# Kernel optimization log

Hardware: AMD Instinct MI355X
Metric: run time of the kernel (lower is better)

## Reference

```python
import jax, jax.numpy as jnp
import numpy as np

N_NODES = 100000
N_EDGES = 1600000
D_FEAT = 64


def setup_inputs() -> dict:
    key = jax.random.key(0)
    k1, k2, k3 = jax.random.split(key, 3)
    features = jax.random.normal(k1, (N_NODES, D_FEAT), dtype=jnp.float32)
    row = jax.random.randint(k2, (N_EDGES,), 0, N_NODES, dtype=jnp.int64 if jax.config.jax_enable_x64 else jnp.int32)
    col = jax.random.randint(k3, (N_EDGES,), 0, N_NODES, dtype=jnp.int64 if jax.config.jax_enable_x64 else jnp.int32)
    return {"features": features, "row": row, "col": col}


def reference(features, row, col):
    # adj @ H  ==  segment-sum of H[col] grouped by row (COO SpMM)
    n = features.shape[0]
    gathered = features[col]                                  # [E, d] irregular gather
    summed = jax.ops.segment_sum(gathered, row, num_segments=n)  # [N, d]
    # deg = clip(adj.sum(1), 1, None) -> per-row nonzero count
    ones = jnp.ones((row.shape[0],), dtype=features.dtype)
    deg = jax.ops.segment_sum(ones, row, num_segments=n)
    deg = jnp.clip(deg, 1.0, None)
    agg = summed / deg[:, None]
    # combine: residual add
    return features + agg
```

## Files before the change

### kernel.cpp

```cpp
#include <hip/hip_runtime.h>

#define D_FEAT 64
#define RB 64
#define RBITS 6
#define CELLCAP 16
#define E_BLK 8192
#define TMAX 256
#define NBMAX2 1600
#define SCAP 2048
#define OVCAP 65536

__device__ inline unsigned short f2bf(float f) {
    unsigned u = __float_as_uint(f);
    u += 0x7FFFu + ((u >> 16) & 1u);
    return (unsigned short)(u >> 16);
}
__device__ inline float bf_lo(unsigned u) { return __uint_as_float(u << 16); }
__device__ inline float bf_hi(unsigned u) { return __uint_as_float(u & 0xFFFF0000u); }

__global__ __launch_bounds__(64)
void zero_kernel(int* __restrict__ p, int n) {
    int i = blockIdx.x * 64 + threadIdx.x;
    if (i < n) p[i] = 0;
}

__global__ __launch_bounds__(256)
void bin2_conv_kernel(const int* __restrict__ row, const int* __restrict__ col,
                      int* __restrict__ cnts,
                      int* __restrict__ slab,
                      int* __restrict__ ovfcnt,
                      int2* __restrict__ ovf,
                      int n_edges, int ebt, int nb,
                      const float* __restrict__ feat, unsigned short* __restrict__ feat_bf,
                      int n4) {
    int gb = blockIdx.x;
    int t = threadIdx.x;
    if (gb < ebt) {
        __shared__ int hist[NBMAX2];
        __shared__ int cur[NBMAX2];
        for (int i = t; i < nb; i += 256) { hist[i] = 0; cur[i] = 0; }
        __syncthreads();
        int e0 = gb * E_BLK, e1 = min(e0 + E_BLK, n_edges);
        for (int e = e0 + t; e < e1; e += 256)
            atomicAdd(&hist[row[e] >> RBITS], 1);
        __syncthreads();
        for (int i = t; i < nb; i += 256)
            cnts[(size_t)gb * nb + i] = hist[i];
        for (int e = e0 + t; e < e1; e += 256) {
            int r = row[e], c = col[e];
            int b = r >> RBITS;
            int pos = atomicAdd(&cur[b], 1);
            if (pos < CELLCAP) {
                slab[((size_t)b * ebt + gb) * CELLCAP + pos] = ((r & (RB - 1)) << 17) | c;
            } else {
                int op = atomicAdd(ovfcnt, 1);
                if (op < OVCAP) ovf[op] = make_int2(r, c);
            }
        }
    } else {
        int i = (gb - ebt) * 256 + t;
        if (i < n4) {
            float4 f = reinterpret_cast<const float4*>(feat)[i];
            ushort4 u;
            u.x = f2bf(f.x); u.y = f2bf(f.y); u.z = f2bf(f.z); u.w = f2bf(f.w);
            reinterpret_cast<ushort4*>(feat_bf)[i] = u;
        }
    }
}

template<int BF>
__global__ __launch_bounds__(256, 6)
void aggregate5_kernel(const float* __restrict__ feat,
                       const unsigned short* __restrict__ feat_bf,
                       const int* __restrict__ slab,
                       const int* __restrict__ cnts,
                       const int* __restrict__ ovfcnt,
                       const int2* __restrict__ ovf,
                       const int* __restrict__ row, const int* __restrict__ col,
                       float* __restrict__ out, int n_nodes, int n_edges,
                       int nb, int ebt) {
    __shared__ int cellc[TMAX];
    __shared__ int scol[SCAP];
    __shared__ int cnt[RB], csum[RB], cur[RB], ddeg[RB];
    __shared__ int sred[256];

    int b = blockIdx.x;
    int t = threadIdx.x;
    int w = t >> 6, lane = t & 63;
    int q = lane >> 3, sub = lane & 7;
    int rA = w * 16 + q;
    int rB = rA + 8;

    for (int i = t; i < ebt; i += 256) cellc[i] = cnts[(size_t)i * nb + b];
    if (t < RB) { cnt[t] = 0; ddeg[t] = 0; }
    __syncthreads();

    int pt = 0;
    for (int i = t; i < ebt; i += 256) pt += cellc[i];
    sred[t] = pt;
    __syncthreads();
    for (int o = 128; o > 0; o >>= 1) {
        if (t < o) sred[t] += sred[t + o];
        __syncthreads();
    }
    int btotal = sred[0];
    int rawoc = *ovfcnt;
    int oc = min(rawoc, OVCAP);
    bool fb = (btotal > SCAP) || (rawoc > OVCAP);

    float acc[16];
    #pragma unroll
    for (int k = 0; k < 16; ++k) acc[k] = 0.f;

#define GATHER(cv, o0)                                                         \
    do {                                                                       \
        if (BF) {                                                              \
            uint4 d = *reinterpret_cast<const uint4*>(                         \
                feat_bf + (size_t)(cv)*D_FEAT + sub * 8);                      \
            acc[o0+0] += bf_lo(d.x); acc[o0+1] += bf_hi(d.x);                  \
            acc[o0+2] += bf_lo(d.y); acc[o0+3] += bf_hi(d.y);                  \
            acc[o0+4] += bf_lo(d.z); acc[o0+5] += bf_hi(d.z);                  \
            acc[o0+6] += bf_lo(d.w); acc[o0+7] += bf_hi(d.w);                  \
        } else {                                                               \
            float4 x0 = *reinterpret_cast<const float4*>(                      \
                feat + (size_t)(cv)*D_FEAT + sub * 8);                         \
            float4 x1 = *reinterpret_cast<const float4*>(                      \
                feat + (size_t)(cv)*D_FEAT + sub * 8 + 4);                     \
            acc[o0+0] += x0.x; acc[o0+1] += x0.y;                              \
            acc[o0+2] += x0.z; acc[o0+3] += x0.w;                              \
            acc[o0+4] += x1.x; acc[o0+5] += x1.y;                              \
            acc[o0+6] += x1.z; acc[o0+7] += x1.w;                              \
        }                                                                      \
    } while (0)

    if (!fb) {
        int nslots = ebt * CELLCAP;
        const int* sp = slab + (size_t)b * nslots;
        for (int i = t; i < nslots; i += 256) {
            int cell = i >> 4, pos = i & 15;
            if (pos < min(cellc[cell], CELLCAP)) {
                int pk = sp[i];
                atomicAdd(&cnt[((unsigned)pk) >> 17], 1);
            }
        }
        for (int i = t; i < oc; i += 256) {
            int2 rc = ovf[i];
            if ((rc.x >> RBITS) == b) atomicAdd(&cnt[rc.x & (RB - 1)], 1);
        }
        __syncthreads();
        if (t < RB) csum[t] = cnt[t];
        __syncthreads();
        for (int o = 1; o < RB; o <<= 1) {
            int v = (t < RB && t >= o) ? csum[t - o] : 0;
            __syncthreads();
            if (t < RB) csum[t] += v;
            __syncthreads();
        }
        if (t < RB) { cur[t] = csum[t] - cnt[t]; ddeg[t] = cnt[t]; }
        __syncthreads();
        for (int i = t; i < nslots; i += 256) {
            int cell = i >> 4, pos = i & 15;
            if (pos < min(cellc[cell], CELLCAP)) {
                int pk = sp[i];
                int lr = ((unsigned)pk) >> 17;
                scol[atomicAdd(&cur[lr], 1)] = pk & 0x1FFFF;
            }
        }
        for (int i = t; i < oc; i += 256) {
            int2 rc = ovf[i];
            if ((rc.x >> RBITS) == b)
                scol[atomicAdd(&cur[rc.x & (RB - 1)], 1)] = rc.y;
        }
        __syncthreads();
        int cA = cnt[rA], sA = csum[rA] - cA;
        int cB = cnt[rB], sB = csum[rB] - cB;
        int m = max(cA, cB);
        for (int j = 0; j < m; ++j) {
            if (j < cA) { int c = scol[sA + j]; GATHER(c, 0); }
            if (j < cB) { int c = scol[sB + j]; GATHER(c, 8); }
        }
    } else {
        for (int base = 0; base < n_edges; base += SCAP) {
            int ce = min(SCAP, n_edges - base);
            if (t < RB) cnt[t] = 0;
            __syncthreads();
            for (int i = t; i < ce; i += 256) {
                int r = row[base + i];
                if ((r >> RBITS) == b) atomicAdd(&cnt[r & (RB - 1)], 1);
            }
            __syncthreads();
            if (t < RB) csum[t] = cnt[t];
            __syncthreads();
            for (int o = 1; o < RB; o <<= 1) {
                int v = (t < RB && t >= o) ? csum[t - o] : 0;
                __syncthreads();
                if (t < RB) csum[t] += v;
                __syncthreads();
            }
            if (t < RB) { cur[t] = csum[t] - cnt[t]; ddeg[t] += cnt[t]; }
            __syncthreads();
            for (int i = t; i < ce; i += 256) {
                int r = row[base + i];
                if ((r >> RBITS) == b)
                    scol[atomicAdd(&cur[r & (RB - 1)], 1)] = col[base + i];
            }
            __syncthreads();
            int cA = cnt[rA], sA = csum[rA] - cA;
            int cB = cnt[rB], sB = csum[rB] - cB;
            int m = max(cA, cB);
            for (int j = 0; j < m; ++j) {
                if (j < cA) { int c = scol[sA + j]; GATHER(c, 0); }
                if (j < cB) { int c = scol[sB + j]; GATHER(c, 8); }
            }
            __syncthreads();
        }
    }
    __syncthreads();

    {
        int r = b * RB + rA;
        if (r < n_nodes) {
            float inv = 1.0f / fmaxf((float)ddeg[rA], 1.0f);
            size_t off = (size_t)r * D_FEAT + sub * 8;
            float4 f0 = *reinterpret_cast<const float4*>(feat + off);
            float4 f1 = *reinterpret_cast<const float4*>(feat + off + 4);
            float4 o0, o1;
            o0.x = f0.x + acc[0] * inv; o0.y = f0.y + acc[1] * inv;
            o0.z = f0.z + acc[2] * inv; o0.w = f0.w + acc[3] * inv;
            o1.x = f1.x + acc[4] * inv; o1.y = f1.y + acc[5] * inv;
            o1.z = f1.z + acc[6] * inv; o1.w = f1.w + acc[7] * inv;
            *reinterpret_cast<float4*>(out + off) = o0;
            *reinterpret_cast<float4*>(out + off + 4) = o1;
        }
        r = b * RB + rB;
        if (r < n_nodes) {
            float inv = 1.0f / fmaxf((float)ddeg[rB], 1.0f);
            size_t off = (size_t)r * D_FEAT + sub * 8;
            float4 f0 = *reinterpret_cast<const float4*>(feat + off);
            float4 f1 = *reinterpret_cast<const float4*>(feat + off + 4);
            float4 o0, o1;
            o0.x = f0.x + acc[8]  * inv; o0.y = f0.y + acc[9]  * inv;
            o0.z = f0.z + acc[10] * inv; o0.w = f0.w + acc[11] * inv;
            o1.x = f1.x + acc[12] * inv; o1.y = f1.y + acc[13] * inv;
            o1.z = f1.z + acc[14] * inv; o1.w = f1.w + acc[15] * inv;
            *reinterpret_cast<float4*>(out + off) = o0;
            *reinterpret_cast<float4*>(out + off + 4) = o1;
        }
    }
#undef GATHER
}

extern "C" void kernel_launch(void* const* d_in, const int* in_sizes, int n_in,
                              void* d_out, int out_size, void* d_ws, size_t ws_size,
                              hipStream_t stream) {
    const float* feat = (const float*)d_in[0];
    const int* row = (const int*)d_in[1];
    const int* col = (const int*)d_in[2];
    float* out = (float*)d_out;

    const int n_nodes = in_sizes[0] / D_FEAT;
    const int n_edges = in_sizes[1];
    const int nb = (n_nodes + RB - 1) / RB;
    const int ebt = (n_edges + E_BLK - 1) / E_BLK;
    const int n4 = n_nodes * D_FEAT / 4;

    size_t slab_bytes = (size_t)nb * ebt * CELLCAP * 4;
    size_t cnts_bytes = (size_t)ebt * nb * 4;
    size_t ovf_bytes  = (size_t)OVCAP * 8;
    size_t bf_bytes   = (size_t)n_nodes * D_FEAT * 2;

    size_t lean_need = slab_bytes + cnts_bytes + ovf_bytes + 512;
    size_t fat_need  = lean_need + ((bf_bytes + 63) & ~(size_t)63);
    bool fat = (ws_size >= fat_need);

    char* ws = (char*)d_ws;
    size_t p = 0;
    int* slab = (int*)(ws + p); p += slab_bytes;
    int* cnts = (int*)(ws + p); p += cnts_bytes;
    int2* ovf = (int2*)(ws + p); p += ovf_bytes;
    int* ovfcnt = (int*)(ws + p); p += 64;
    p = (p + 63) & ~(size_t)63;
    unsigned short* feat_bf = nullptr;
    if (fat) { feat_bf = (unsigned short*)(ws + p); }

    zero_kernel<<<1, 64, 0, stream>>>(ovfcnt, 1);

    {
        int conv_blocks = fat ? (n4 + 255) / 256 : 0;
        bin2_conv_kernel<<<ebt + conv_blocks, 256, 0, stream>>>(
            row, col, cnts, slab, ovfcnt, ovf, n_edges, ebt, nb,
            feat, feat_bf, fat ? n4 : 0);
    }
    if (fat) {
        aggregate5_kernel<1><<<nb, 256, 0, stream>>>(
            feat, feat_bf, slab, cnts, ovfcnt, ovf, row, col,
            out, n_nodes, n_edges, nb, ebt);
    } else {
        aggregate5_kernel<0><<<nb, 256, 0, stream>>>(
            feat, nullptr, slab, cnts, ovfcnt, ovf, row, col,
            out, n_nodes, n_edges, nb, ebt);
    }
}
```

Measured before the change: 151.8 us.

## Drop binning histogram pass and balance row gathers across edges with shuffle reduction

The binning kernel now runs 1024 threads per block and uses its final per-bin cursor values as the cell counts, which removes the separate histogram pass over row indices. The aggregate kernel moves to 512 threads. Each wave now processes one row at a time, with 8 lane groups splitting that row's edges and combining partial sums through cross-lane shuffles. The previous scheme gave each thread group fixed rows and iterated to the larger row degree. The new mapping targets load imbalance between rows and lets each row issue more gathers in parallel, at the cost of shuffle reductions and a larger block. The fallback path now accumulates in the output buffer across chunks.

```diff
diff --git a/kernel.cpp b/kernel.cpp
--- a/kernel.cpp
+++ b/kernel.cpp
@@ -24,8 +24,8 @@
     if (i < n) p[i] = 0;
 }
 
-__global__ __launch_bounds__(256)
-void bin2_conv_kernel(const int* __restrict__ row, const int* __restrict__ col,
+__global__ __launch_bounds__(1024)
+void bin3_conv_kernel(const int* __restrict__ row, const int* __restrict__ col,
                       int* __restrict__ cnts,
                       int* __restrict__ slab,
                       int* __restrict__ ovfcnt,
@@ -36,17 +36,11 @@
     int gb = blockIdx.x;
     int t = threadIdx.x;
     if (gb < ebt) {
-        __shared__ int hist[NBMAX2];
         __shared__ int cur[NBMAX2];
-        for (int i = t; i < nb; i += 256) { hist[i] = 0; cur[i] = 0; }
+        for (int i = t; i < nb; i += 1024) cur[i] = 0;
         __syncthreads();
         int e0 = gb * E_BLK, e1 = min(e0 + E_BLK, n_edges);
-        for (int e = e0 + t; e < e1; e += 256)
-            atomicAdd(&hist[row[e] >> RBITS], 1);
-        __syncthreads();
-        for (int i = t; i < nb; i += 256)
-            cnts[(size_t)gb * nb + i] = hist[i];
-        for (int e = e0 + t; e < e1; e += 256) {
+        for (int e = e0 + t; e < e1; e += 1024) {
             int r = row[e], c = col[e];
             int b = r >> RBITS;
             int pos = atomicAdd(&cur[b], 1);
@@ -57,8 +51,11 @@
                 if (op < OVCAP) ovf[op] = make_int2(r, c);
             }
         }
+        __syncthreads();
+        for (int i = t; i < nb; i += 1024)
+            cnts[(size_t)gb * nb + i] = cur[i];
     } else {
-        int i = (gb - ebt) * 256 + t;
+        int i = (gb - ebt) * 1024 + t;
         if (i < n4) {
             float4 f = reinterpret_cast<const float4*>(feat)[i];
             ushort4 u;
@@ -69,8 +66,8 @@
 }
 
 template<int BF>
-__global__ __launch_bounds__(256, 6)
-void aggregate5_kernel(const float* __restrict__ feat,
+__global__ __launch_bounds__(512, 4)
+void aggregate6_kernel(const float* __restrict__ feat,
                        const unsigned short* __restrict__ feat_bf,
                        const int* __restrict__ slab,
                        const int* __restrict__ cnts,
@@ -82,24 +79,22 @@
     __shared__ int cellc[TMAX];
     __shared__ int scol[SCAP];
     __shared__ int cnt[RB], csum[RB], cur[RB], ddeg[RB];
-    __shared__ int sred[256];
+    __shared__ int sred[512];
 
     int b = blockIdx.x;
     int t = threadIdx.x;
     int w = t >> 6, lane = t & 63;
     int q = lane >> 3, sub = lane & 7;
-    int rA = w * 16 + q;
-    int rB = rA + 8;
-
-    for (int i = t; i < ebt; i += 256) cellc[i] = cnts[(size_t)i * nb + b];
+
+    for (int i = t; i < ebt; i += 512) cellc[i] = cnts[(size_t)i * nb + b];
     if (t < RB) { cnt[t] = 0; ddeg[t] = 0; }
     __syncthreads();
 
     int pt = 0;
-    for (int i = t; i < ebt; i += 256) pt += cellc[i];
+    for (int i = t; i < ebt; i += 512) pt += cellc[i];
     sred[t] = pt;
     __syncthreads();
-    for (int o = 128; o > 0; o >>= 1) {
+    for (int o = 256; o > 0; o >>= 1) {
         if (t < o) sred[t] += sred[t + o];
         __syncthreads();
     }
@@ -108,84 +103,115 @@
     int oc = min(rawoc, OVCAP);
     bool fb = (btotal > SCAP) || (rawoc > OVCAP);
 
-    float acc[16];
-    #pragma unroll
-    for (int k = 0; k < 16; ++k) acc[k] = 0.f;
-
-#define GATHER(cv, o0)                                                         \
+#define GATHER(cv, A)                                                          \
     do {                                                                       \
         if (BF) {                                                              \
             uint4 d = *reinterpret_cast<const uint4*>(                         \
                 feat_bf + (size_t)(cv)*D_FEAT + sub * 8);                      \
-            acc[o0+0] += bf_lo(d.x); acc[o0+1] += bf_hi(d.x);                  \
-            acc[o0+2] += bf_lo(d.y); acc[o0+3] += bf_hi(d.y);                  \
-            acc[o0+4] += bf_lo(d.z); acc[o0+5] += bf_hi(d.z);                  \
-            acc[o0+6] += bf_lo(d.w); acc[o0+7] += bf_hi(d.w);                  \
+            A[0] += bf_lo(d.x); A[1] += bf_hi(d.x);                            \
+            A[2] += bf_lo(d.y); A[3] += bf_hi(d.y);                            \
+            A[4] += bf_lo(d.z); A[5] += bf_hi(d.z);                            \
+            A[6] += bf_lo(d.w); A[7] += bf_hi(d.w);                            \
         } else {                                                               \
             float4 x0 = *reinterpret_cast<const float4*>(                      \
                 feat + (size_t)(cv)*D_FEAT + sub * 8);                         \
             float4 x1 = *reinterpret_cast<const float4*>(                      \
                 feat + (size_t)(cv)*D_FEAT + sub * 8 + 4);                     \
-            acc[o0+0] += x0.x; acc[o0+1] += x0.y;                              \
-            acc[o0+2] += x0.z; acc[o0+3] += x0.w;                              \
-            acc[o0+4] += x1.x; acc[o0+5] += x1.y;                              \
-            acc[o0+6] += x1.z; acc[o0+7] += x1.w;                              \
+            A[0] += x0.x; A[1] += x0.y; A[2] += x0.z; A[3] += x0.w;            \
+            A[4] += x1.x; A[5] += x1.y; A[6] += x1.z; A[7] += x1.w;            \
         }                                                                      \
     } while (0)
 
     if (!fb) {
         int nslots = ebt * CELLCAP;
         const int* sp = slab + (size_t)b * nslots;
-        for (int i = t; i < nslots; i += 256) {
+        for (int i = t; i < nslots; i += 512) {
+            int cell = i >> 4, pos = i & 15;
+            if (pos < min(cellc[cell], CELLCAP))
+                atomicAdd(&cnt[((unsigned)sp[i]) >> 17], 1);
+        }
+        for (int i = t; i < oc; i += 512) {
+            int2 rc = ovf[i];
+            if ((rc.x >> RBITS) == b) atomicAdd(&cnt[rc.x & (RB - 1)], 1);
+        }
+        __syncthreads();
+        if (t < RB) csum[t] = cnt[t];
+        __syncthreads();
+        for (int o = 1; o < RB; o <<= 1) {
+            int v = (t < RB && t >= o) ? csum[t - o] : 0;
+            __syncthreads();
+            if (t < RB) csum[t] += v;
+            __syncthreads();
+        }
+        if (t < RB) cur[t] = csum[t] - cnt[t];
+        __syncthreads();
+        for (int i = t; i < nslots; i += 512) {
             int cell = i >> 4, pos = i & 15;
             if (pos < min(cellc[cell], CELLCAP)) {
                 int pk = sp[i];
-                atomicAdd(&cnt[((unsigned)pk) >> 17], 1);
-            }
-        }
-        for (int i = t; i < oc; i += 256) {
-            int2 rc = ovf[i];
-            if ((rc.x >> RBITS) == b) atomicAdd(&cnt[rc.x & (RB - 1)], 1);
-        }
-        __syncthreads();
-        if (t < RB) csum[t] = cnt[t];
-        __syncthreads();
-        for (int o = 1; o < RB; o <<= 1) {
-            int v = (t < RB && t >= o) ? csum[t - o] : 0;
-            __syncthreads();
-            if (t < RB) csum[t] += v;
-            __syncthreads();
-        }
-        if (t < RB) { cur[t] = csum[t] - cnt[t]; ddeg[t] = cnt[t]; }
-        __syncthreads();
-        for (int i = t; i < nslots; i += 256) {
-            int cell = i >> 4, pos = i & 15;
-            if (pos < min(cellc[cell], CELLCAP)) {
-                int pk = sp[i];
-                int lr = ((unsigned)pk) >> 17;
-                scol[atomicAdd(&cur[lr], 1)] = pk & 0x1FFFF;
-            }
-        }
-        for (int i = t; i < oc; i += 256) {
+                scol[atomicAdd(&cur[((unsigned)pk) >> 17], 1)] = pk & 0x1FFFF;
+            }
+        }
+        for (int i = t; i < oc; i += 512) {
             int2 rc = ovf[i];
             if ((rc.x >> RBITS) == b)
                 scol[atomicAdd(&cur[rc.x & (RB - 1)], 1)] = rc.y;
         }
         __syncthreads();
-        int cA = cnt[rA], sA = csum[rA] - cA;
-        int cB = cnt[rB], sB = csum[rB] - cB;
-        int m = max(cA, cB);
-        for (int j = 0; j < m; ++j) {
-            if (j < cA) { int c = scol[sA + j]; GATHER(c, 0); }
-            if (j < cB) { int c = scol[sB + j]; GATHER(c, 8); }
+        #pragma unroll 2
+        for (int rr = 0; rr < 8; ++rr) {
+            int lr = w + rr * 8;
+            int r = b * RB + lr;
+            if (r >= n_nodes) continue;
+            int deg = cnt[lr];
+            int s0 = csum[lr] - deg;
+            float a0[8], a1[8];
+            #pragma unroll
+            for (int k = 0; k < 8; ++k) { a0[k] = 0.f; a1[k] = 0.f; }
+            for (int base = 0; base < deg; base += 16) {
+                int j0 = base + q, j1 = base + 8 + q;
+                int c0 = (j0 < deg) ? scol[s0 + j0] : -1;
+                int c1 = (j1 < deg) ? scol[s0 + j1] : -1;
+                if (c0 >= 0) GATHER(c0, a0);
+                if (c1 >= 0) GATHER(c1, a1);
+            }
+            #pragma unroll
+            for (int k = 0; k < 8; ++k) a0[k] += a1[k];
+            #pragma unroll
+            for (int k = 0; k < 8; ++k) {
+                a0[k] += __shfl_xor(a0[k], 8, 64);
+                a0[k] += __shfl_xor(a0[k], 16, 64);
+                a0[k] += __shfl_xor(a0[k], 32, 64);
+            }
+            if (q == 0) {
+                float inv = 1.0f / fmaxf((float)deg, 1.0f);
+                size_t off = (size_t)r * D_FEAT + sub * 8;
+                float4 f0 = *reinterpret_cast<const float4*>(feat + off);
+                float4 f1 = *reinterpret_cast<const float4*>(feat + off + 4);
+                float4 o0, o1;
+                o0.x = f0.x + a0[0] * inv; o0.y = f0.y + a0[1] * inv;
+                o0.z = f0.z + a0[2] * inv; o0.w = f0.w + a0[3] * inv;
+                o1.x = f1.x + a0[4] * inv; o1.y = f1.y + a0[5] * inv;
+                o1.z = f1.z + a0[6] * inv; o1.w = f1.w + a0[7] * inv;
+                *reinterpret_cast<float4*>(out + off) = o0;
+                *reinterpret_cast<float4*>(out + off + 4) = o1;
+            }
         }
     } else {
-        for (int base = 0; base < n_edges; base += SCAP) {
-            int ce = min(SCAP, n_edges - base);
+        for (int j = t; j < RB * 16; j += 512) {
+            int lr = j >> 4, r = b * RB + lr;
+            if (r < n_nodes) {
+                float4 z = make_float4(0.f, 0.f, 0.f, 0.f);
+                *reinterpret_cast<float4*>(out + (size_t)r * D_FEAT + (j & 15) * 4) = z;
+            }
+        }
+        __syncthreads();
+        for (int base0 = 0; base0 < n_edges; base0 += SCAP) {
+            int ce = min(SCAP, n_edges - base0);
             if (t < RB) cnt[t] = 0;
             __syncthreads();
-            for (int i = t; i < ce; i += 256) {
-                int r = row[base + i];
+            for (int i = t; i < ce; i += 512) {
+                int r = row[base0 + i];
                 if ((r >> RBITS) == b) atomicAdd(&cnt[r & (RB - 1)], 1);
             }
             __syncthreads();
@@ -199,52 +225,61 @@
             }
             if (t < RB) { cur[t] = csum[t] - cnt[t]; ddeg[t] += cnt[t]; }
             __syncthreads();
-            for (int i = t; i < ce; i += 256) {
-                int r = row[base + i];
+            for (int i = t; i < ce; i += 512) {
+                int r = row[base0 + i];
                 if ((r >> RBITS) == b)
-                    scol[atomicAdd(&cur[r & (RB - 1)], 1)] = col[base + i];
-            }
-            __syncthreads();
-            int cA = cnt[rA], sA = csum[rA] - cA;
-            int cB = cnt[rB], sB = csum[rB] - cB;
-            int m = max(cA, cB);
-            for (int j = 0; j < m; ++j) {
-                if (j < cA) { int c = scol[sA + j]; GATHER(c, 0); }
-                if (j < cB) { int c = scol[sB + j]; GATHER(c, 8); }
-            }
-            __syncthreads();
-        }
-    }
-    __syncthreads();
-
-    {
-        int r = b * RB + rA;
-        if (r < n_nodes) {
-            float inv = 1.0f / fmaxf((float)ddeg[rA], 1.0f);
-            size_t off = (size_t)r * D_FEAT + sub * 8;
-            float4 f0 = *reinterpret_cast<const float4*>(feat + off);
-            float4 f1 = *reinterpret_cast<const float4*>(feat + off + 4);
-            float4 o0, o1;
-            o0.x = f0.x + acc[0] * inv; o0.y = f0.y + acc[1] * inv;
-            o0.z = f0.z + acc[2] * inv; o0.w = f0.w + acc[3] * inv;
-            o1.x = f1.x + acc[4] * inv; o1.y = f1.y + acc[5] * inv;
-            o1.z = f1.z + acc[6] * inv; o1.w = f1.w + acc[7] * inv;
-            *reinterpret_cast<float4*>(out + off) = o0;
-            *reinterpret_cast<float4*>(out + off + 4) = o1;
-        }
-        r = b * RB + rB;
-        if (r < n_nodes) {
-            float inv = 1.0f / fmaxf((float)ddeg[rB], 1.0f);
-            size_t off = (size_t)r * D_FEAT + sub * 8;
-            float4 f0 = *reinterpret_cast<const float4*>(feat + off);
-            float4 f1 = *reinterpret_cast<const float4*>(feat + off + 4);
-            float4 o0, o1;
-            o0.x = f0.x + acc[8]  * inv; o0.y = f0.y + acc[9]  * inv;
-            o0.z = f0.z + acc[10] * inv; o0.w = f0.w + acc[11] * inv;
-            o1.x = f1.x + acc[12] * inv; o1.y = f1.y + acc[13] * inv;
-            o1.z = f1.z + acc[14] * inv; o1.w = f1.w + acc[15] * inv;
-            *reinterpret_cast<float4*>(out + off) = o0;
-            *reinterpret_cast<float4*>(out + off + 4) = o1;
+                    scol[atomicAdd(&cur[r & (RB - 1)], 1)] = col[base0 + i];
+            }
+            __syncthreads();
+            for (int rr = 0; rr < 8; ++rr) {
+                int lr = w + rr * 8;
+                int r = b * RB + lr;
+                if (r >= n_nodes) continue;
+                int deg = cnt[lr];
+                int s0 = csum[lr] - deg;
+                float a0[8], a1[8];
+                #pragma unroll
+                for (int k = 0; k < 8; ++k) { a0[k] = 0.f; a1[k] = 0.f; }
+                for (int base = 0; base < deg; base += 16) {
+                    int j0 = base + q, j1 = base + 8 + q;
+                    int c0 = (j0 < deg) ? scol[s0 + j0] : -1;
+                    int c1 = (j1 < deg) ? scol[s0 + j1] : -1;
+                    if (c0 >= 0) GATHER(c0, a0);
+                    if (c1 >= 0) GATHER(c1, a1);
+                }
+                #pragma unroll
+                for (int k = 0; k < 8; ++k) a0[k] += a1[k];
+                #pragma unroll
+                for (int k = 0; k < 8; ++k) {
+                    a0[k] += __shfl_xor(a0[k], 8, 64);
+                    a0[k] += __shfl_xor(a0[k], 16, 64);
+                    a0[k] += __shfl_xor(a0[k], 32, 64);
+                }
+                if (q == 0) {
+                    size_t off = (size_t)r * D_FEAT + sub * 8;
+                    float4 s0v = *reinterpret_cast<const float4*>(out + off);
+                    float4 s1v = *reinterpret_cast<const float4*>(out + off + 4);
+                    s0v.x += a0[0]; s0v.y += a0[1]; s0v.z += a0[2]; s0v.w += a0[3];
+                    s1v.x += a0[4]; s1v.y += a0[5]; s1v.z += a0[6]; s1v.w += a0[7];
+                    *reinterpret_cast<float4*>(out + off) = s0v;
+                    *reinterpret_cast<float4*>(out + off + 4) = s1v;
+                }
+            }
+            __syncthreads();
+        }
+        for (int j = t; j < RB * 16; j += 512) {
+            int lr = j >> 4, r = b * RB + lr;
+            if (r < n_nodes) {
+                int f = (j & 15) * 4;
+                float inv = 1.0f / fmaxf((float)ddeg[lr], 1.0f);
+                size_t off = (size_t)r * D_FEAT + f;
+                float4 s = *reinterpret_cast<const float4*>(out + off);
+                float4 fv = *reinterpret_cast<const float4*>(feat + off);
+                float4 o;
+                o.x = fv.x + s.x * inv; o.y = fv.y + s.y * inv;
+                o.z = fv.z + s.z * inv; o.w = fv.w + s.w * inv;
+                *reinterpret_cast<float4*>(out + off) = o;
+            }
         }
     }
 #undef GATHER
@@ -286,17 +321,17 @@
     zero_kernel<<<1, 64, 0, stream>>>(ovfcnt, 1);
 
     {
-        int conv_blocks = fat ? (n4 + 255) / 256 : 0;
-        bin2_conv_kernel<<<ebt + conv_blocks, 256, 0, stream>>>(
+        int conv_blocks = fat ? (n4 + 1023) / 1024 : 0;
+        bin3_conv_kernel<<<ebt + conv_blocks, 1024, 0, stream>>>(
             row, col, cnts, slab, ovfcnt, ovf, n_edges, ebt, nb,
             feat, feat_bf, fat ? n4 : 0);
     }
     if (fat) {
-        aggregate5_kernel<1><<<nb, 256, 0, stream>>>(
+        aggregate6_kernel<1><<<nb, 512, 0, stream>>>(
             feat, feat_bf, slab, cnts, ovfcnt, ovf, row, col,
             out, n_nodes, n_edges, nb, ebt);
     } else {
-        aggregate5_kernel<0><<<nb, 256, 0, stream>>>(
+        aggregate6_kernel<0><<<nb, 512, 0, stream>>>(
             feat, nullptr, slab, cnts, ovfcnt, ovf, row, col,
             out, n_nodes, n_edges, nb, ebt);
     }
```

Measured after the change: 158.4 us. 4.3% more time.

## Replace fixed-capacity slab binning with per-tile sorted buffers and prefix offsets

Applied to the files above, without the earlier changes.

The binning kernel now sorts each 8192-edge tile by 256-row bucket in shared memory and writes the tile contiguously with per-bucket prefix offsets, replacing the fixed-cap slab cells, overflow list and zero kernel. The aggregate kernel uses 1024-thread blocks covering 256 rows, reads each tile's contiguous segment, and loops over chunks of the shared column buffer in place of the separate full-edge-scan fallback. This removes the overflow atomics, one kernel launch and padded slab reads. In exchange it uses much larger shared memory per block, fewer and bigger blocks (about 391), and requires extra chunk passes when a bucket exceeds the buffer.

```diff
diff --git a/kernel.cpp b/kernel.cpp
--- a/kernel.cpp
+++ b/kernel.cpp
@@ -1,14 +1,12 @@
 #include <hip/hip_runtime.h>
 
 #define D_FEAT 64
-#define RB 64
-#define RBITS 6
-#define CELLCAP 16
+#define CB 256
+#define CBITS 8
+#define NB2MAX 512
 #define E_BLK 8192
 #define TMAX 256
-#define NBMAX2 1600
-#define SCAP 2048
-#define OVCAP 65536
+#define SCAP 4608
 
 __device__ inline unsigned short f2bf(float f) {
     unsigned u = __float_as_uint(f);
@@ -18,47 +16,60 @@
 __device__ inline float bf_lo(unsigned u) { return __uint_as_float(u << 16); }
 __device__ inline float bf_hi(unsigned u) { return __uint_as_float(u & 0xFFFF0000u); }
 
-__global__ __launch_bounds__(64)
-void zero_kernel(int* __restrict__ p, int n) {
-    int i = blockIdx.x * 64 + threadIdx.x;
-    if (i < n) p[i] = 0;
-}
-
-__global__ __launch_bounds__(256)
-void bin2_conv_kernel(const int* __restrict__ row, const int* __restrict__ col,
-                      int* __restrict__ cnts,
-                      int* __restrict__ slab,
-                      int* __restrict__ ovfcnt,
-                      int2* __restrict__ ovf,
-                      int n_edges, int ebt, int nb,
-                      const float* __restrict__ feat, unsigned short* __restrict__ feat_bf,
-                      int n4) {
+__global__ __launch_bounds__(1024, 4)
+void bin5_conv_kernel(const int* __restrict__ row, const int* __restrict__ col,
+                      int* __restrict__ tilebuf,
+                      int* __restrict__ csumG,
+                      int n_edges, int ebt, int nb2,
+                      const float* __restrict__ feat,
+                      unsigned short* __restrict__ feat_bf, int n4) {
     int gb = blockIdx.x;
     int t = threadIdx.x;
     if (gb < ebt) {
-        __shared__ int hist[NBMAX2];
-        __shared__ int cur[NBMAX2];
-        for (int i = t; i < nb; i += 256) { hist[i] = 0; cur[i] = 0; }
+        __shared__ int hist[NB2MAX];
+        __shared__ int scn[NB2MAX];
+        __shared__ int ebuf[E_BLK];
+        for (int i = t; i < nb2; i += 1024) hist[i] = 0;
         __syncthreads();
         int e0 = gb * E_BLK, e1 = min(e0 + E_BLK, n_edges);
-        for (int e = e0 + t; e < e1; e += 256)
-            atomicAdd(&hist[row[e] >> RBITS], 1);
-        __syncthreads();
-        for (int i = t; i < nb; i += 256)
-            cnts[(size_t)gb * nb + i] = hist[i];
-        for (int e = e0 + t; e < e1; e += 256) {
-            int r = row[e], c = col[e];
-            int b = r >> RBITS;
-            int pos = atomicAdd(&cur[b], 1);
-            if (pos < CELLCAP) {
-                slab[((size_t)b * ebt + gb) * CELLCAP + pos] = ((r & (RB - 1)) << 17) | c;
-            } else {
-                int op = atomicAdd(ovfcnt, 1);
-                if (op < OVCAP) ovf[op] = make_int2(r, c);
+        int ne = e1 - e0;
+        int rr[8], cc[8];
+        #pragma unroll
+        for (int k = 0; k < 8; ++k) {
+            int i = t + k * 1024;
+            if (i < ne) { rr[k] = row[e0 + i]; cc[k] = col[e0 + i]; }
+            else rr[k] = -1;
+        }
+        #pragma unroll
+        for (int k = 0; k < 8; ++k)
+            if (rr[k] >= 0) atomicAdd(&hist[rr[k] >> CBITS], 1);
+        __syncthreads();
+        if (t < nb2) scn[t] = hist[t];
+        __syncthreads();
+        for (int o = 1; o < nb2; o <<= 1) {
+            int v = (t < nb2 && t >= o) ? scn[t - o] : 0;
+            __syncthreads();
+            if (t < nb2) scn[t] += v;
+            __syncthreads();
+        }
+        if (t < nb2) hist[t] = scn[t] - hist[t];
+        __syncthreads();
+        for (int i = t; i < nb2 + 1; i += 1024)
+            csumG[(size_t)gb * (nb2 + 1) + i] = (i < nb2) ? hist[i] : ne;
+        __syncthreads();
+        #pragma unroll
+        for (int k = 0; k < 8; ++k) {
+            if (rr[k] >= 0) {
+                int b = rr[k] >> CBITS;
+                int pos = atomicAdd(&hist[b], 1);
+                ebuf[pos] = ((rr[k] & (CB - 1)) << 17) | cc[k];
             }
         }
+        __syncthreads();
+        for (int i = t; i < ne; i += 1024)
+            tilebuf[(size_t)gb * E_BLK + i] = ebuf[i];
     } else {
-        int i = (gb - ebt) * 256 + t;
+        int i = (gb - ebt) * 1024 + t;
         if (i < n4) {
             float4 f = reinterpret_cast<const float4*>(feat)[i];
             ushort4 u;
@@ -69,44 +80,39 @@
 }
 
 template<int BF>
-__global__ __launch_bounds__(256, 6)
-void aggregate5_kernel(const float* __restrict__ feat,
-                       const unsigned short* __restrict__ feat_bf,
-                       const int* __restrict__ slab,
-                       const int* __restrict__ cnts,
-                       const int* __restrict__ ovfcnt,
-                       const int2* __restrict__ ovf,
-                       const int* __restrict__ row, const int* __restrict__ col,
-                       float* __restrict__ out, int n_nodes, int n_edges,
-                       int nb, int ebt) {
-    __shared__ int cellc[TMAX];
+__global__ __launch_bounds__(1024, 8)
+void agg7_kernel(const float* __restrict__ feat,
+                 const unsigned short* __restrict__ feat_bf,
+                 const int* __restrict__ tilebuf,
+                 const int* __restrict__ csumG,
+                 float* __restrict__ out, int n_nodes, int ebt, int nb2) {
+    __shared__ int tstart[TMAX], tlen[TMAX], psum[TMAX];
     __shared__ int scol[SCAP];
-    __shared__ int cnt[RB], csum[RB], cur[RB], ddeg[RB];
-    __shared__ int sred[256];
-
-    int b = blockIdx.x;
+    __shared__ int cnt[CB], csum[CB], cur[CB], ddeg[CB];
+
+    int cb = blockIdx.x;
     int t = threadIdx.x;
     int w = t >> 6, lane = t & 63;
     int q = lane >> 3, sub = lane & 7;
     int rA = w * 16 + q;
     int rB = rA + 8;
 
-    for (int i = t; i < ebt; i += 256) cellc[i] = cnts[(size_t)i * nb + b];
-    if (t < RB) { cnt[t] = 0; ddeg[t] = 0; }
+    for (int i = t; i < ebt; i += 1024) {
+        int s = csumG[(size_t)i * (nb2 + 1) + cb];
+        int e = csumG[(size_t)i * (nb2 + 1) + cb + 1];
+        tstart[i] = s; tlen[i] = e - s;
+    }
+    if (t < CB) ddeg[t] = 0;
     __syncthreads();
-
-    int pt = 0;
-    for (int i = t; i < ebt; i += 256) pt += cellc[i];
-    sred[t] = pt;
+    if (t < ebt) psum[t] = tlen[t];
     __syncthreads();
-    for (int o = 128; o > 0; o >>= 1) {
-        if (t < o) sred[t] += sred[t + o];
-        __syncthreads();
-    }
-    int btotal = sred[0];
-    int rawoc = *ovfcnt;
-    int oc = min(rawoc, OVCAP);
-    bool fb = (btotal > SCAP) || (rawoc > OVCAP);
+    for (int o = 1; o < ebt; o <<= 1) {
+        int v = (t < ebt && t >= o) ? psum[t - o] : 0;
+        __syncthreads();
+        if (t < ebt) psum[t] += v;
+        __syncthreads();
+    }
+    int total = psum[ebt - 1];
 
     float acc[16];
     #pragma unroll
@@ -133,92 +139,52 @@
         }                                                                      \
     } while (0)
 
-    if (!fb) {
-        int nslots = ebt * CELLCAP;
-        const int* sp = slab + (size_t)b * nslots;
-        for (int i = t; i < nslots; i += 256) {
-            int cell = i >> 4, pos = i & 15;
-            if (pos < min(cellc[cell], CELLCAP)) {
-                int pk = sp[i];
-                atomicAdd(&cnt[((unsigned)pk) >> 17], 1);
+    for (int L = 0; L < total; L += SCAP) {
+        int R = min(L + SCAP, total);
+        if (t < CB) cnt[t] = 0;
+        __syncthreads();
+        for (int tt = w; tt < ebt; tt += 16) {
+            int pre = psum[tt] - tlen[tt];
+            int lo = max(L - pre, 0), hi = min(tlen[tt], R - pre);
+            const int* tp = tilebuf + (size_t)tt * E_BLK + tstart[tt];
+            for (int i = lo + lane; i < hi; i += 64)
+                atomicAdd(&cnt[((unsigned)tp[i]) >> 17], 1);
+        }
+        __syncthreads();
+        if (t < CB) csum[t] = cnt[t];
+        __syncthreads();
+        for (int o = 1; o < CB; o <<= 1) {
+            int v = (t < CB && t >= o) ? csum[t - o] : 0;
+            __syncthreads();
+            if (t < CB) csum[t] += v;
+            __syncthreads();
+        }
+        if (t < CB) { cur[t] = csum[t] - cnt[t]; ddeg[t] += cnt[t]; }
+        __syncthreads();
+        for (int tt = w; tt < ebt; tt += 16) {
+            int pre = psum[tt] - tlen[tt];
+            int lo = max(L - pre, 0), hi = min(tlen[tt], R - pre);
+            const int* tp = tilebuf + (size_t)tt * E_BLK + tstart[tt];
+            for (int i = lo + lane; i < hi; i += 64) {
+                int pk = tp[i];
+                scol[atomicAdd(&cur[((unsigned)pk) >> 17], 1)] = pk & 0x1FFFF;
             }
         }
-        for (int i = t; i < oc; i += 256) {
-            int2 rc = ovf[i];
-            if ((rc.x >> RBITS) == b) atomicAdd(&cnt[rc.x & (RB - 1)], 1);
-        }
-        __syncthreads();
-        if (t < RB) csum[t] = cnt[t];
-        __syncthreads();
-        for (int o = 1; o < RB; o <<= 1) {
-            int v = (t < RB && t >= o) ? csum[t - o] : 0;
-            __syncthreads();
-            if (t < RB) csum[t] += v;
-            __syncthreads();
-        }
-        if (t < RB) { cur[t] = csum[t] - cnt[t]; ddeg[t] = cnt[t]; }
-        __syncthreads();
-        for (int i = t; i < nslots; i += 256) {
-            int cell = i >> 4, pos = i & 15;
-            if (pos < min(cellc[cell], CELLCAP)) {
-                int pk = sp[i];
-                int lr = ((unsigned)pk) >> 17;
-                scol[atomicAdd(&cur[lr], 1)] = pk & 0x1FFFF;
-            }
-        }
-        for (int i = t; i < oc; i += 256) {
-            int2 rc = ovf[i];
-            if ((rc.x >> RBITS) == b)
-                scol[atomicAdd(&cur[rc.x & (RB - 1)], 1)] = rc.y;
-        }
         __syncthreads();
         int cA = cnt[rA], sA = csum[rA] - cA;
-        int cB = cnt[rB], sB = csum[rB] - cB;
-        int m = max(cA, cB);
+        int cB2 = cnt[rB], sB = csum[rB] - cB2;
+        int m = max(cA, cB2);
+        #pragma unroll 2
         for (int j = 0; j < m; ++j) {
             if (j < cA) { int c = scol[sA + j]; GATHER(c, 0); }
-            if (j < cB) { int c = scol[sB + j]; GATHER(c, 8); }
-        }
-    } else {
-        for (int base = 0; base < n_edges; base += SCAP) {
-            int ce = min(SCAP, n_edges - base);
-            if (t < RB) cnt[t] = 0;
-            __syncthreads();
-            for (int i = t; i < ce; i += 256) {
-                int r = row[base + i];
-                if ((r >> RBITS) == b) atomicAdd(&cnt[r & (RB - 1)], 1);
-            }
-            __syncthreads();
-            if (t < RB) csum[t] = cnt[t];
-            __syncthreads();
-            for (int o = 1; o < RB; o <<= 1) {
-                int v = (t < RB && t >= o) ? csum[t - o] : 0;
-                __syncthreads();
-                if (t < RB) csum[t] += v;
-                __syncthreads();
-            }
-            if (t < RB) { cur[t] = csum[t] - cnt[t]; ddeg[t] += cnt[t]; }
-            __syncthreads();
-            for (int i = t; i < ce; i += 256) {
-                int r = row[base + i];
-                if ((r >> RBITS) == b)
-                    scol[atomicAdd(&cur[r & (RB - 1)], 1)] = col[base + i];
-            }
-            __syncthreads();
-            int cA = cnt[rA], sA = csum[rA] - cA;
-            int cB = cnt[rB], sB = csum[rB] - cB;
-            int m = max(cA, cB);
-            for (int j = 0; j < m; ++j) {
-                if (j < cA) { int c = scol[sA + j]; GATHER(c, 0); }
-                if (j < cB) { int c = scol[sB + j]; GATHER(c, 8); }
-            }
-            __syncthreads();
-        }
-    }
-    __syncthreads();
+            if (j < cB2) { int c = scol[sB + j]; GATHER(c, 8); }
+        }
+        __syncthreads();
+    }
+#undef GATHER
 
     {
-        int r = b * RB + rA;
+        int r = cb * CB + rA;
         if (r < n_nodes) {
             float inv = 1.0f / fmaxf((float)ddeg[rA], 1.0f);
             size_t off = (size_t)r * D_FEAT + sub * 8;
@@ -232,7 +198,7 @@
             *reinterpret_cast<float4*>(out + off) = o0;
             *reinterpret_cast<float4*>(out + off + 4) = o1;
         }
-        r = b * RB + rB;
+        r = cb * CB + rB;
         if (r < n_nodes) {
             float inv = 1.0f / fmaxf((float)ddeg[rB], 1.0f);
             size_t off = (size_t)r * D_FEAT + sub * 8;
@@ -247,7 +213,6 @@
             *reinterpret_cast<float4*>(out + off + 4) = o1;
         }
     }
-#undef GATHER
 }
 
 extern "C" void kernel_launch(void* const* d_in, const int* in_sizes, int n_in,
@@ -260,44 +225,37 @@
 
     const int n_nodes = in_sizes[0] / D_FEAT;
     const int n_edges = in_sizes[1];
-    const int nb = (n_nodes + RB - 1) / RB;
+    const int nb2 = (n_nodes + CB - 1) / CB;
     const int ebt = (n_edges + E_BLK - 1) / E_BLK;
     const int n4 = n_nodes * D_FEAT / 4;
 
-    size_t slab_bytes = (size_t)nb * ebt * CELLCAP * 4;
-    size_t cnts_bytes = (size_t)ebt * nb * 4;
-    size_t ovf_bytes  = (size_t)OVCAP * 8;
-    size_t bf_bytes   = (size_t)n_nodes * D_FEAT * 2;
-
-    size_t lean_need = slab_bytes + cnts_bytes + ovf_bytes + 512;
+    size_t tb_bytes  = (size_t)ebt * E_BLK * 4;
+    size_t cs_bytes  = (size_t)ebt * (nb2 + 1) * 4;
+    size_t bf_bytes  = (size_t)n_nodes * D_FEAT * 2;
+
+    size_t lean_need = tb_bytes + cs_bytes + 256;
     size_t fat_need  = lean_need + ((bf_bytes + 63) & ~(size_t)63);
     bool fat = (ws_size >= fat_need);
 
     char* ws = (char*)d_ws;
     size_t p = 0;
-    int* slab = (int*)(ws + p); p += slab_bytes;
-    int* cnts = (int*)(ws + p); p += cnts_bytes;
-    int2* ovf = (int2*)(ws + p); p += ovf_bytes;
-    int* ovfcnt = (int*)(ws + p); p += 64;
+    int* tilebuf = (int*)(ws + p); p += tb_bytes;
+    int* csumG   = (int*)(ws + p); p += cs_bytes;
     p = (p + 63) & ~(size_t)63;
     unsigned short* feat_bf = nullptr;
     if (fat) { feat_bf = (unsigned short*)(ws + p); }
 
-    zero_kernel<<<1, 64, 0, stream>>>(ovfcnt, 1);
-
     {
-        int conv_blocks = fat ? (n4 + 255) / 256 : 0;
-        bin2_conv_kernel<<<ebt + conv_blocks, 256, 0, stream>>>(
-            row, col, cnts, slab, ovfcnt, ovf, n_edges, ebt, nb,
+        int conv_blocks = fat ? (n4 + 1023) / 1024 : 0;
+        bin5_conv_kernel<<<ebt + conv_blocks, 1024, 0, stream>>>(
+            row, col, tilebuf, csumG, n_edges, ebt, nb2,
             feat, feat_bf, fat ? n4 : 0);
     }
     if (fat) {
-        aggregate5_kernel<1><<<nb, 256, 0, stream>>>(
-            feat, feat_bf, slab, cnts, ovfcnt, ovf, row, col,
-            out, n_nodes, n_edges, nb, ebt);
+        agg7_kernel<1><<<nb2, 1024, 0, stream>>>(
+            feat, feat_bf, tilebuf, csumG, out, n_nodes, ebt, nb2);
     } else {
-        aggregate5_kernel<0><<<nb, 256, 0, stream>>>(
-            feat, nullptr, slab, cnts, ovfcnt, ovf, row, col,
-            out, n_nodes, n_edges, nb, ebt);
-    }
-}
+        agg7_kernel<0><<<nb2, 1024, 0, stream>>>(
+            feat, nullptr, tilebuf, csumG, out, n_nodes, ebt, nb2);
+    }
+}
```

Result: faster. 134.7 us (-11.2%).
